# Kernel tuning notes

Hardware: AMD Instinct MI355X
Metric: run time of the kernel (lower is better)

## Reference

```python
import jax, jax.numpy as jnp
import numpy as np

HIDDEN = 1024
HEADS = 16
HEAD_DIM = HIDDEN // HEADS  # 64
B, S = 4, 2048


def setup_inputs() -> dict:
    key = jax.random.key(0)
    ks = jax.random.split(key, 9)
    sd = 1.0 / np.sqrt(HIDDEN)
    return {
        "hidden_state": jax.random.normal(ks[0], (B, S, HIDDEN), dtype=jnp.float32),
        "Wq": jax.random.uniform(ks[1], (HIDDEN, HIDDEN), jnp.float32, -sd, sd),
        "bq": jax.random.uniform(ks[2], (HIDDEN,), jnp.float32, -sd, sd),
        "Wk": jax.random.uniform(ks[3], (HIDDEN, HEAD_DIM), jnp.float32, -sd, sd),
        "bk": jax.random.uniform(ks[4], (HEAD_DIM,), jnp.float32, -sd, sd),
        "Wv": jax.random.uniform(ks[5], (HIDDEN, HEAD_DIM), jnp.float32, -sd, sd),
        "bv": jax.random.uniform(ks[6], (HEAD_DIM,), jnp.float32, -sd, sd),
        "Wo": jax.random.uniform(ks[7], (HIDDEN, HIDDEN), jnp.float32, -sd, sd),
        "bo": jax.random.uniform(ks[8], (HIDDEN,), jnp.float32, -sd, sd),
    }


def reference(hidden_state, Wq, bq, Wk, bk, Wv, bv, Wo, bo):
    b, s, _ = hidden_state.shape
    # projections
    q = hidden_state @ Wq + bq               # [B,S,H*Dh]
    k = hidden_state @ Wk + bk               # [B,S,Dh] (shared across heads)
    v = hidden_state @ Wv + bv               # [B,S,Dh]
    q = q.reshape(b, s, HEADS, HEAD_DIM)     # [B,S,H,Dh]
    scale = 1.0 / jnp.sqrt(jnp.float32(HEAD_DIM))
    # scores: [B,H,S,S] — shared K broadcast over heads via einsum
    scores = jnp.einsum("bqhd,bkd->bhqk", q, k) * scale
    probs = jax.nn.softmax(scores, axis=-1)
    out = jnp.einsum("bhqk,bkd->bqhd", probs, v)  # [B,S,H,Dh]
    out = out.reshape(b, s, HEADS * HEAD_DIM)
    return out @ Wo + bo
```

## Files before the change

kernel.cpp:

```cpp
#include <hip/hip_runtime.h>
#include <hip/hip_bf16.h>
#include <cstdint>

#define HIDDEN 1024
#define HEADS 16
#define HEAD_DIM 64
#define BB 4
#define SS 2048
#define NTOK (BB * SS)

typedef __attribute__((ext_vector_type(8))) __bf16 bf16x8;
typedef __attribute__((ext_vector_type(4))) float f32x4;
typedef unsigned short u16;

#define PSCALE 0.1803368801111137f

__device__ __forceinline__ u16 f2bf(float x) {
    union { float f; uint32_t u; } v; v.f = x;
    uint32_t r = v.u + 0x7FFF + ((v.u >> 16) & 1);
    return (u16)(r >> 16);
}

typedef __attribute__((address_space(3))) uint32_t lds_u32;
typedef __attribute__((address_space(1))) uint32_t glb_u32;
__device__ __forceinline__ void gload16(const u16* g, u16* l) {
    __builtin_amdgcn_global_load_lds((const glb_u32*)g, (lds_u32*)l, 16, 0, 0);
}

__global__ void cvt_f32_bf16(const float* __restrict__ in, u16* __restrict__ out, int n4) {
    int i = blockIdx.x * blockDim.x + threadIdx.x;
    int stride = gridDim.x * blockDim.x;
    for (; i < n4; i += stride) {
        float4 v = ((const float4*)in)[i];
        ushort4 o;
        o.x = f2bf(v.x); o.y = f2bf(v.y); o.z = f2bf(v.z); o.w = f2bf(v.w);
        ((ushort4*)out)[i] = o;
    }
}

__global__ void transpose_to_bf16(const float* __restrict__ W, u16* __restrict__ Wt,
                                  int K, int N) {
    __shared__ float tile[32][33];
    int bx = blockIdx.x;
    int by = blockIdx.y;
    int tx = threadIdx.x;
    int ty = threadIdx.y;
    for (int i = 0; i < 4; i++) {
        int kk = ty + i * 8;
        tile[kk][tx] = W[(size_t)(by * 32 + kk) * N + bx * 32 + tx];
    }
    __syncthreads();
    for (int i = 0; i < 4; i++) {
        int nn = ty + i * 8;
        Wt[(size_t)(bx * 32 + nn) * K + by * 32 + tx] = f2bf(tile[tx][nn]);
    }
}

__global__ __launch_bounds__(256) void gemm128_f32(
    const u16* __restrict__ A, const u16* __restrict__ Bt,
    const float* __restrict__ bias, float* __restrict__ C,
    int M, int N, int K) {
    __shared__ u16 Al[128 * 64];
    __shared__ u16 Bl[128 * 64];
    const int mb = blockIdx.y, nb = blockIdx.x;
    const int tid = threadIdx.x;
    const int w = tid >> 6, lane = tid & 63;
    const int lr = lane & 15, lg = lane >> 4;
    const int wr = w >> 1, wc = w & 1;

    f32x4 acc[4][4] = {};

    const int srow = lane >> 3;
    const int scol = (lane & 7) * 8;
    const u16* Asrc = A + (size_t)(mb * 128 + w * 32 + srow) * K + scol;
    const u16* Bsrc = Bt + (size_t)(nb * 128 + w * 32 + srow) * K + scol;
    u16* Adst = &Al[(w * 32) * 64];
    u16* Bdst = &Bl[(w * 32) * 64];

    for (int k0 = 0; k0 < K; k0 += 64) {
        if (k0) __syncthreads();
#pragma unroll
        for (int i = 0; i < 4; i++) {
            gload16(Asrc + (size_t)(i * 8) * K + k0, Adst + i * 8 * 64);
            gload16(Bsrc + (size_t)(i * 8) * K + k0, Bdst + i * 8 * 64);
        }
        asm volatile("s_waitcnt vmcnt(0)" ::: "memory");
        __syncthreads();

#pragma unroll
        for (int ks = 0; ks < 2; ks++) {
            bf16x8 af[4], bfr[4];
#pragma unroll
            for (int mf = 0; mf < 4; mf++)
                af[mf] = *(const bf16x8*)(&Al[(wr * 64 + mf * 16 + lr) * 64 + ks * 32 + lg * 8]);
#pragma unroll
            for (int nf = 0; nf < 4; nf++)
                bfr[nf] = *(const bf16x8*)(&Bl[(wc * 64 + nf * 16 + lr) * 64 + ks * 32 + lg * 8]);
            __builtin_amdgcn_s_setprio(1);
#pragma unroll
            for (int mf = 0; mf < 4; mf++)
#pragma unroll
                for (int nf = 0; nf < 4; nf++)
                    acc[mf][nf] = __builtin_amdgcn_mfma_f32_16x16x32_bf16(af[mf], bfr[nf], acc[mf][nf], 0, 0, 0);
            __builtin_amdgcn_s_setprio(0);
        }
    }

#pragma unroll
    for (int nf = 0; nf < 4; nf++) {
        int n = nb * 128 + wc * 64 + nf * 16 + lr;
        float bval = bias[n];
#pragma unroll
        for (int mf = 0; mf < 4; mf++)
#pragma unroll
            for (int r = 0; r < 4; r++) {
                int m = mb * 128 + wr * 64 + mf * 16 + lg * 4 + r;
                C[(size_t)m * N + n] = acc[mf][nf][r] + bval;
            }
    }
}

#define NPROJ 1152
__global__ __launch_bounds__(256) void gemm_proj(
    const u16* __restrict__ A, const u16* __restrict__ Bt,
    const float* __restrict__ bq, const float* __restrict__ bk, const float* __restrict__ bv,
    u16* __restrict__ qout, u16* __restrict__ kout, u16* __restrict__ vout) {
    __shared__ u16 Al[128 * 64];
    __shared__ u16 Bl[128 * 64];
    const int mb = blockIdx.y, nb = blockIdx.x;
    const int tid = threadIdx.x;
    const int w = tid >> 6, lane = tid & 63;
    const int lr = lane & 15, lg = lane >> 4;
    const int wr = w >> 1, wc = w & 1;

    f32x4 acc[4][4] = {};

    const int srow = lane >> 3;
    const int scol = (lane & 7) * 8;
    const u16* Asrc = A + (size_t)(mb * 128 + w * 32 + srow) * HIDDEN + scol;
    const u16* Bsrc = Bt + (size_t)(nb * 128 + w * 32 + srow) * HIDDEN + scol;
    u16* Adst = &Al[(w * 32) * 64];
    u16* Bdst = &Bl[(w * 32) * 64];

    for (int k0 = 0; k0 < HIDDEN; k0 += 64) {
        if (k0) __syncthreads();
#pragma unroll
        for (int i = 0; i < 4; i++) {
            gload16(Asrc + (size_t)(i * 8) * HIDDEN + k0, Adst + i * 8 * 64);
            gload16(Bsrc + (size_t)(i * 8) * HIDDEN + k0, Bdst + i * 8 * 64);
        }
        asm volatile("s_waitcnt vmcnt(0)" ::: "memory");
        __syncthreads();

#pragma unroll
        for (int ks = 0; ks < 2; ks++) {
            bf16x8 af[4], bfr[4];
#pragma unroll
            for (int mf = 0; mf < 4; mf++)
                af[mf] = *(const bf16x8*)(&Al[(wr * 64 + mf * 16 + lr) * 64 + ks * 32 + lg * 8]);
#pragma unroll
            for (int nf = 0; nf < 4; nf++)
                bfr[nf] = *(const bf16x8*)(&Bl[(wc * 64 + nf * 16 + lr) * 64 + ks * 32 + lg * 8]);
            __builtin_amdgcn_s_setprio(1);
#pragma unroll
            for (int mf = 0; mf < 4; mf++)
#pragma unroll
                for (int nf = 0; nf < 4; nf++)
                    acc[mf][nf] = __builtin_amdgcn_mfma_f32_16x16x32_bf16(af[mf], bfr[nf], acc[mf][nf], 0, 0, 0);
            __builtin_amdgcn_s_setprio(0);
        }
    }

#pragma unroll
    for (int nf = 0; nf < 4; nf++) {
        int n = nb * 128 + wc * 64 + nf * 16 + lr;
        float bval = (n < 1024) ? bq[n] : (n < 1088) ? bk[n - 1024] : bv[n - 1088];
#pragma unroll
        for (int mf = 0; mf < 4; mf++)
#pragma unroll
            for (int r = 0; r < 4; r++) {
                int m = mb * 128 + wr * 64 + mf * 16 + lg * 4 + r;
                float val = acc[mf][nf][r] + bval;
                if (n < 1024) {
                    qout[(size_t)m * 1024 + n] = f2bf(val * PSCALE);
                } else if (n < 1088) {
                    kout[(size_t)m * 64 + (n - 1024)] = f2bf(val);
                } else {
                    int bb = m >> 11, t = m & (SS - 1);
                    vout[((size_t)bb * 64 + (n - 1088)) * SS + t] = f2bf(val);
                }
            }
    }
}

#define KVB 64
#define NT (SS / KVB)

__global__ __launch_bounds__(512) void attn_kernel(
    const u16* __restrict__ q,
    const u16* __restrict__ k,
    const u16* __restrict__ vt,
    u16* __restrict__ o) {
    const int qt = blockIdx.x, h = blockIdx.y, b = blockIdx.z;
    const int tid = threadIdx.x;
    const int w = tid >> 6, lane = tid & 63;
    const int lr = lane & 15, lg = lane >> 4;

    __shared__ u16 Kl[4][KVB * 64];
    __shared__ u16 Vl[4][KVB * 64];

    const u16* kbase = k + (size_t)b * SS * HEAD_DIM;
    const u16* vbase = vt + (size_t)b * HEAD_DIM * SS;
    const int rowbase = b * SS + qt * 256 + w * 32;

    const int srow = w * 8 + (lane >> 3);
    const int sc16 = (lane & 7) ^ (srow & 7);
    const u16* kp = kbase + (size_t)srow * HEAD_DIM + sc16 * 8;
    const u16* vp = vbase + (size_t)srow * SS + sc16 * 8;

    bf16x8 qf[2][2];
#pragma unroll
    for (int s = 0; s < 2; s++)
#pragma unroll
        for (int ks = 0; ks < 2; ks++)
            qf[s][ks] = *(const bf16x8*)(q + (size_t)(rowbase + s * 16 + lr) * HIDDEN + h * 64 + ks * 32 + lg * 8);

    bf16x8 onesf;
#pragma unroll
    for (int i = 0; i < 8; i++) onesf[i] = (__bf16)1.0f;

    const int xr = lr & 7;
    const int kvro0 = lr * 64 + ((lg) ^ xr) * 8;
    const int kvro1 = lr * 64 + ((4 + lg) ^ xr) * 8;

    f32x4 l_acc[2] = {};
    f32x4 oacc[2][4] = {};

#define VEXP(D, S) asm("v_exp_f32 %0, %1" : "=v"(D) : "v"(S))

#define STAGE(BUF)                            \
    do {                                      \
        gload16(kp, &Kl[BUF][w * 512]);       \
        gload16(vp, &Vl[BUF][w * 512]);       \
        kp += KVB * HEAD_DIM;                 \
        vp += KVB;                            \
    } while (0)

#define CTILE(BUF)                                                                     \
    do {                                                                               \
        f32x4 st0[4] = {}, st1[4] = {};                                                \
        __builtin_amdgcn_s_setprio(1);                                                 \
        _Pragma("unroll") for (int nf = 0; nf < 4; nf++) {                             \
            bf16x8 kf = *(const bf16x8*)(&Kl[BUF][kvro0 + nf * 1024]);                 \
            st0[nf] = __builtin_amdgcn_mfma_f32_16x16x32_bf16(kf, qf[0][0], st0[nf], 0, 0, 0); \
            st1[nf] = __builtin_amdgcn_mfma_f32_16x16x32_bf16(kf, qf[1][0], st1[nf], 0, 0, 0); \
        }                                                                              \
        _Pragma("unroll") for (int nf = 0; nf < 4; nf++) {                             \
            bf16x8 kf = *(const bf16x8*)(&Kl[BUF][kvro1 + nf * 1024]);                 \
            st0[nf] = __builtin_amdgcn_mfma_f32_16x16x32_bf16(kf, qf[0][1], st0[nf], 0, 0, 0); \
            st1[nf] = __builtin_amdgcn_mfma_f32_16x16x32_bf16(kf, qf[1][1], st1[nf], 0, 0, 0); \
        }                                                                              \
        __builtin_amdgcn_s_setprio(0);                                                 \
                      \
        uint32_t c0[8], c1[8];                                                         \
        _Pragma("unroll") for (int nf = 0; nf < 4; nf++) {                             \
            float p0, p1, p2, p3, r0, r1, r2, r3;                                      \
            VEXP(p0, st0[nf][0]); VEXP(p1, st0[nf][1]);                                \
            VEXP(p2, st0[nf][2]); VEXP(p3, st0[nf][3]);                                \
            asm("v_cvt_pk_bf16_f32 %0, %1, %2" : "=v"(c0[nf * 2]) : "v"(p0), "v"(p1)); \
            asm("v_cvt_pk_bf16_f32 %0, %1, %2" : "=v"(c0[nf * 2 + 1]) : "v"(p2), "v"(p3)); \
            VEXP(r0, st1[nf][0]); VEXP(r1, st1[nf][1]);                                \
            VEXP(r2, st1[nf][2]); VEXP(r3, st1[nf][3]);                                \
            asm("v_cvt_pk_bf16_f32 %0, %1, %2" : "=v"(c1[nf * 2]) : "v"(r0), "v"(r1)); \
            asm("v_cvt_pk_bf16_f32 %0, %1, %2" : "=v"(c1[nf * 2 + 1]) : "v"(r2), "v"(r3)); \
        }                                                                              \
                                              \
        _Pragma("unroll") for (int ks = 0; ks < 2; ks++) {                             \
            uint32_t u0 = c0[4 * ks], v0 = c0[4 * ks + 1], x0 = c0[4 * ks + 2], y0 = c0[4 * ks + 3]; \
            uint32_t u1 = c1[4 * ks], v1 = c1[4 * ks + 1], x1 = c1[4 * ks + 2], y1 = c1[4 * ks + 3]; \
            asm("v_permlane32_swap_b32 %0, %1" : "+v"(u0), "+v"(x0));                  \
            asm("v_permlane32_swap_b32 %0, %1" : "+v"(v0), "+v"(y0));                  \
            asm("v_permlane16_swap_b32 %0, %1" : "+v"(u0), "+v"(x0));                  \
            asm("v_permlane16_swap_b32 %0, %1" : "+v"(v0), "+v"(y0));                  \
            asm("v_permlane32_swap_b32 %0, %1" : "+v"(u1), "+v"(x1));                  \
            asm("v_permlane32_swap_b32 %0, %1" : "+v"(v1), "+v"(y1));                  \
            asm("v_permlane16_swap_b32 %0, %1" : "+v"(u1), "+v"(x1));                  \
            asm("v_permlane16_swap_b32 %0, %1" : "+v"(v1), "+v"(y1));                  \
            union { uint32_t wv[4]; bf16x8 v8; } pf0, pf1;                             \
            pf0.wv[0] = u0; pf0.wv[1] = v0; pf0.wv[2] = x0; pf0.wv[3] = y0;            \
            pf1.wv[0] = u1; pf1.wv[1] = v1; pf1.wv[2] = x1; pf1.wv[3] = y1;            \
            const int kvro = ks ? kvro1 : kvro0;                                       \
            __builtin_amdgcn_s_setprio(1);                                             \
            l_acc[0] = __builtin_amdgcn_mfma_f32_16x16x32_bf16(pf0.v8, onesf, l_acc[0], 0, 0, 0); \
            l_acc[1] = __builtin_amdgcn_mfma_f32_16x16x32_bf16(pf1.v8, onesf, l_acc[1], 0, 0, 0); \
            _Pragma("unroll") for (int nf = 0; nf < 4; nf++) {                         \
                bf16x8 vf = *(const bf16x8*)(&Vl[BUF][kvro + nf * 1024]);              \
                oacc[0][nf] = __builtin_amdgcn_mfma_f32_16x16x32_bf16(pf0.v8, vf, oacc[0][nf], 0, 0, 0); \
                oacc[1][nf] = __builtin_amdgcn_mfma_f32_16x16x32_bf16(pf1.v8, vf, oacc[1][nf], 0, 0, 0); \
            }                                                                          \
            __builtin_amdgcn_s_setprio(0);                                             \
        }                                                                              \
    } while (0)

#define STEP(BUFC, DOSTAGE, VM)                                    \
    do {                                                           \
        asm volatile("s_waitcnt vmcnt(" #VM ")" ::: "memory");     \
        __builtin_amdgcn_s_barrier();                              \
        if (DOSTAGE) STAGE(((BUFC) + 3) & 3);                      \
        CTILE(BUFC);                                               \
        asm volatile("" ::: "memory");                             \
    } while (0)

    STAGE(0);
    STAGE(1);
    STAGE(2);

    for (int i = 0; i < 7; i++) {
        STEP(0, 1, 4);
        STEP(1, 1, 4);
        STEP(2, 1, 4);
        STEP(3, 1, 4);
    }
    STEP(0, 1, 4);
    STEP(1, 0, 4);
    STEP(2, 0, 2);
    STEP(3, 0, 0);

#undef STEP
#undef STAGE
#undef CTILE
#undef VEXP

#pragma unroll
    for (int s = 0; s < 2; s++) {
        float li[4];
#pragma unroll
        for (int r = 0; r < 4; r++) li[r] = 1.0f / l_acc[s][r];
#pragma unroll
        for (int nf = 0; nf < 4; nf++)
#pragma unroll
            for (int r = 0; r < 4; r++) {
                float val = oacc[s][nf][r] * li[r];
                o[(size_t)(rowbase + s * 16 + lg * 4 + r) * HIDDEN + h * 64 + nf * 16 + lr] = f2bf(val);
            }
    }
}

extern "C" void kernel_launch(void* const* d_in, const int* in_sizes, int n_in,
                              void* d_out, int out_size, void* d_ws, size_t ws_size,
                              hipStream_t stream) {
    const float* h  = (const float*)d_in[0];
    const float* Wq = (const float*)d_in[1];
    const float* bq = (const float*)d_in[2];
    const float* Wk = (const float*)d_in[3];
    const float* bk = (const float*)d_in[4];
    const float* Wv = (const float*)d_in[5];
    const float* bv = (const float*)d_in[6];
    const float* Wo = (const float*)d_in[7];
    const float* bo = (const float*)d_in[8];

    char* ws = (char*)d_ws;
    u16* hbf  = (u16*)ws; ws += (size_t)NTOK * HIDDEN * 2;
    u16* Wta  = (u16*)ws; ws += (size_t)NPROJ * HIDDEN * 2;
    u16* Wot  = (u16*)ws; ws += (size_t)HIDDEN * HIDDEN * 2;
    u16* qbf  = (u16*)ws; ws += (size_t)NTOK * HIDDEN * 2;
    u16* kbf  = (u16*)ws; ws += (size_t)NTOK * HEAD_DIM * 2;
    u16* vtb  = (u16*)ws; ws += (size_t)NTOK * HEAD_DIM * 2;
    u16* obf  = (u16*)ws; ws += (size_t)NTOK * HIDDEN * 2;

    cvt_f32_bf16<<<2048, 256, 0, stream>>>(h, hbf, NTOK * HIDDEN / 4);
    transpose_to_bf16<<<dim3(HIDDEN / 32, HIDDEN / 32), dim3(32, 8), 0, stream>>>(Wq, Wta, HIDDEN, HIDDEN);
    transpose_to_bf16<<<dim3(HEAD_DIM / 32, HIDDEN / 32), dim3(32, 8), 0, stream>>>(Wk, Wta + (size_t)1024 * HIDDEN, HIDDEN, HEAD_DIM);
    transpose_to_bf16<<<dim3(HEAD_DIM / 32, HIDDEN / 32), dim3(32, 8), 0, stream>>>(Wv, Wta + (size_t)1088 * HIDDEN, HIDDEN, HEAD_DIM);
    transpose_to_bf16<<<dim3(HIDDEN / 32, HIDDEN / 32), dim3(32, 8), 0, stream>>>(Wo, Wot, HIDDEN, HIDDEN);

    gemm_proj<<<dim3(NPROJ / 128, NTOK / 128), 256, 0, stream>>>(hbf, Wta, bq, bk, bv, qbf, kbf, vtb);

    attn_kernel<<<dim3(SS / 256, HEADS, BB), 512, 0, stream>>>(qbf, kbf, vtb, obf);

    gemm128_f32<<<dim3(HIDDEN / 128, NTOK / 128), 256, 0, stream>>>(obf, Wot, bo, (float*)d_out, NTOK, HIDDEN, HIDDEN);
}
```

Before: 152.6 us.

## Pipeline GEMM K-loop with 4-stage LDS ring and swizzled layout

Both GEMM kernels now share a macro-based main loop. It uses a 4-buffer LDS ring with K-step 32, keeps three stages of global-to-LDS loads in flight, and waits on partial vmcnt counts instead of draining after every tile. The LDS layout is XOR-swizzled to cut bank conflicts on the fragment reads. The grid is also transposed so consecutive blocks walk along M, which changes which tiles share L2. The aim is to hide global load latency behind MFMA work, at the cost of more LDS per block and a single barrier per step that relies on the ring depth for safety.

```diff
diff --git a/kernel.cpp b/kernel.cpp
--- a/kernel.cpp
+++ b/kernel.cpp
@@ -56,56 +56,76 @@
     }
 }
 
+
+#define GEMM_PRE()                                                                   \
+    __shared__ u16 Al[4][4096];                                                      \
+    __shared__ u16 Bl[4][4096];                                                      \
+    const int mb = blockIdx.x, nb = blockIdx.y;                                      \
+    const int tid = threadIdx.x;                                                     \
+    const int w = tid >> 6, lane = tid & 63;                                         \
+    const int lr = lane & 15, lg = lane >> 4;                                        \
+    const int wr = w >> 1, wc = w & 1;                                               \
+    f32x4 acc[4][4] = {};                                                            \
+    const int srow4 = lane >> 2;                                                     \
+    const int sg = ((lane & 3) ^ (srow4 & 3)) * 8;                                   \
+    const u16* Ap = A + (size_t)(mb * 128 + w * 32 + srow4) * 1024 + sg;             \
+    const u16* Bp = Bt + (size_t)(nb * 128 + w * 32 + srow4) * 1024 + sg;            \
+    const int aoff = (wr * 64 + lr) * 32 + ((lg ^ (lr & 3)) * 8);                    \
+    const int boff = (wc * 64 + lr) * 32 + ((lg ^ (lr & 3)) * 8);
+
+#define GSTAGE(BUF)                                          \
+    do {                                                     \
+        gload16(Ap, &Al[BUF][w * 1024]);                     \
+        gload16(Ap + 16 * 1024, &Al[BUF][w * 1024 + 512]);   \
+        gload16(Bp, &Bl[BUF][w * 1024]);                     \
+        gload16(Bp + 16 * 1024, &Bl[BUF][w * 1024 + 512]);   \
+        Ap += 32;                                            \
+        Bp += 32;                                            \
+    } while (0)
+
+#define GCOMPUTE(BUF)                                                                \
+    do {                                                                             \
+        bf16x8 af[4], bfr[4];                                                        \
+        _Pragma("unroll") for (int mf = 0; mf < 4; mf++)                             \
+            af[mf] = *(const bf16x8*)(&Al[BUF][aoff + mf * 512]);                    \
+        _Pragma("unroll") for (int nf = 0; nf < 4; nf++)                             \
+            bfr[nf] = *(const bf16x8*)(&Bl[BUF][boff + nf * 512]);                   \
+        __builtin_amdgcn_s_setprio(1);                                               \
+        _Pragma("unroll") for (int mf = 0; mf < 4; mf++)                             \
+            _Pragma("unroll") for (int nf = 0; nf < 4; nf++)                         \
+                acc[mf][nf] = __builtin_amdgcn_mfma_f32_16x16x32_bf16(af[mf], bfr[nf], acc[mf][nf], 0, 0, 0); \
+        __builtin_amdgcn_s_setprio(0);                                               \
+    } while (0)
+
+#define GSTEP(BUFC, DOSTAGE, VM)                                   \
+    do {                                                           \
+        asm volatile("s_waitcnt vmcnt(" #VM ")" ::: "memory");     \
+        __builtin_amdgcn_s_barrier();                              \
+        if (DOSTAGE) GSTAGE(((BUFC) + 3) & 3);                     \
+        GCOMPUTE(BUFC);                                            \
+        asm volatile("" ::: "memory");                             \
+    } while (0)
+
+#define GEMM_LOOP()                                                \
+    GSTAGE(0);                                                     \
+    GSTAGE(1);                                                     \
+    GSTAGE(2);                                                     \
+    for (int i = 0; i < 7; i++) {                                  \
+        GSTEP(0, 1, 8);                                            \
+        GSTEP(1, 1, 8);                                            \
+        GSTEP(2, 1, 8);                                            \
+        GSTEP(3, 1, 8);                                            \
+    }                                                              \
+    GSTEP(0, 1, 8);                                                \
+    GSTEP(1, 0, 8);                                                \
+    GSTEP(2, 0, 4);                                                \
+    GSTEP(3, 0, 0);
+
 __global__ __launch_bounds__(256) void gemm128_f32(
     const u16* __restrict__ A, const u16* __restrict__ Bt,
-    const float* __restrict__ bias, float* __restrict__ C,
-    int M, int N, int K) {
-    __shared__ u16 Al[128 * 64];
-    __shared__ u16 Bl[128 * 64];
-    const int mb = blockIdx.y, nb = blockIdx.x;
-    const int tid = threadIdx.x;
-    const int w = tid >> 6, lane = tid & 63;
-    const int lr = lane & 15, lg = lane >> 4;
-    const int wr = w >> 1, wc = w & 1;
-
-    f32x4 acc[4][4] = {};
-
-    const int srow = lane >> 3;
-    const int scol = (lane & 7) * 8;
-    const u16* Asrc = A + (size_t)(mb * 128 + w * 32 + srow) * K + scol;
-    const u16* Bsrc = Bt + (size_t)(nb * 128 + w * 32 + srow) * K + scol;
-    u16* Adst = &Al[(w * 32) * 64];
-    u16* Bdst = &Bl[(w * 32) * 64];
-
-    for (int k0 = 0; k0 < K; k0 += 64) {
-        if (k0) __syncthreads();
-#pragma unroll
-        for (int i = 0; i < 4; i++) {
-            gload16(Asrc + (size_t)(i * 8) * K + k0, Adst + i * 8 * 64);
-            gload16(Bsrc + (size_t)(i * 8) * K + k0, Bdst + i * 8 * 64);
-        }
-        asm volatile("s_waitcnt vmcnt(0)" ::: "memory");
-        __syncthreads();
-
-#pragma unroll
-        for (int ks = 0; ks < 2; ks++) {
-            bf16x8 af[4], bfr[4];
-#pragma unroll
-            for (int mf = 0; mf < 4; mf++)
-                af[mf] = *(const bf16x8*)(&Al[(wr * 64 + mf * 16 + lr) * 64 + ks * 32 + lg * 8]);
-#pragma unroll
-            for (int nf = 0; nf < 4; nf++)
-                bfr[nf] = *(const bf16x8*)(&Bl[(wc * 64 + nf * 16 + lr) * 64 + ks * 32 + lg * 8]);
-            __builtin_amdgcn_s_setprio(1);
-#pragma unroll
-            for (int mf = 0; mf < 4; mf++)
-#pragma unroll
-                for (int nf = 0; nf < 4; nf++)
-                    acc[mf][nf] = __builtin_amdgcn_mfma_f32_16x16x32_bf16(af[mf], bfr[nf], acc[mf][nf], 0, 0, 0);
-            __builtin_amdgcn_s_setprio(0);
-        }
-    }
-
+    const float* __restrict__ bias, float* __restrict__ C, int N) {
+    GEMM_PRE();
+    GEMM_LOOP();
 #pragma unroll
     for (int nf = 0; nf < 4; nf++) {
         int n = nb * 128 + wc * 64 + nf * 16 + lr;
@@ -120,57 +140,12 @@
     }
 }
 
-#define NPROJ 1152
 __global__ __launch_bounds__(256) void gemm_proj(
     const u16* __restrict__ A, const u16* __restrict__ Bt,
     const float* __restrict__ bq, const float* __restrict__ bk, const float* __restrict__ bv,
     u16* __restrict__ qout, u16* __restrict__ kout, u16* __restrict__ vout) {
-    __shared__ u16 Al[128 * 64];
-    __shared__ u16 Bl[128 * 64];
-    const int mb = blockIdx.y, nb = blockIdx.x;
-    const int tid = threadIdx.x;
-    const int w = tid >> 6, lane = tid & 63;
-    const int lr = lane & 15, lg = lane >> 4;
-    const int wr = w >> 1, wc = w & 1;
-
-    f32x4 acc[4][4] = {};
-
-    const int srow = lane >> 3;
-    const int scol = (lane & 7) * 8;
-    const u16* Asrc = A + (size_t)(mb * 128 + w * 32 + srow) * HIDDEN + scol;
-    const u16* Bsrc = Bt + (size_t)(nb * 128 + w * 32 + srow) * HIDDEN + scol;
-    u16* Adst = &Al[(w * 32) * 64];
-    u16* Bdst = &Bl[(w * 32) * 64];
-
-    for (int k0 = 0; k0 < HIDDEN; k0 += 64) {
-        if (k0) __syncthreads();
-#pragma unroll
-        for (int i = 0; i < 4; i++) {
-            gload16(Asrc + (size_t)(i * 8) * HIDDEN + k0, Adst + i * 8 * 64);
-            gload16(Bsrc + (size_t)(i * 8) * HIDDEN + k0, Bdst + i * 8 * 64);
-        }
-        asm volatile("s_waitcnt vmcnt(0)" ::: "memory");
-        __syncthreads();
-
-#pragma unroll
-        for (int ks = 0; ks < 2; ks++) {
-            bf16x8 af[4], bfr[4];
-#pragma unroll
-            for (int mf = 0; mf < 4; mf++)
-                af[mf] = *(const bf16x8*)(&Al[(wr * 64 + mf * 16 + lr) * 64 + ks * 32 + lg * 8]);
-#pragma unroll
-            for (int nf = 0; nf < 4; nf++)
-                bfr[nf] = *(const bf16x8*)(&Bl[(wc * 64 + nf * 16 + lr) * 64 + ks * 32 + lg * 8]);
-            __builtin_amdgcn_s_setprio(1);
-#pragma unroll
-            for (int mf = 0; mf < 4; mf++)
-#pragma unroll
-                for (int nf = 0; nf < 4; nf++)
-                    acc[mf][nf] = __builtin_amdgcn_mfma_f32_16x16x32_bf16(af[mf], bfr[nf], acc[mf][nf], 0, 0, 0);
-            __builtin_amdgcn_s_setprio(0);
-        }
-    }
-
+    GEMM_PRE();
+    GEMM_LOOP();
 #pragma unroll
     for (int nf = 0; nf < 4; nf++) {
         int n = nb * 128 + wc * 64 + nf * 16 + lr;
@@ -361,7 +336,7 @@
 
     char* ws = (char*)d_ws;
     u16* hbf  = (u16*)ws; ws += (size_t)NTOK * HIDDEN * 2;
-    u16* Wta  = (u16*)ws; ws += (size_t)NPROJ * HIDDEN * 2;
+    u16* Wta  = (u16*)ws; ws += (size_t)1152 * HIDDEN * 2;
     u16* Wot  = (u16*)ws; ws += (size_t)HIDDEN * HIDDEN * 2;
     u16* qbf  = (u16*)ws; ws += (size_t)NTOK * HIDDEN * 2;
     u16* kbf  = (u16*)ws; ws += (size_t)NTOK * HEAD_DIM * 2;
@@ -374,9 +349,9 @@
     transpose_to_bf16<<<dim3(HEAD_DIM / 32, HIDDEN / 32), dim3(32, 8), 0, stream>>>(Wv, Wta + (size_t)1088 * HIDDEN, HIDDEN, HEAD_DIM);
     transpose_to_bf16<<<dim3(HIDDEN / 32, HIDDEN / 32), dim3(32, 8), 0, stream>>>(Wo, Wot, HIDDEN, HIDDEN);
 
-    gemm_proj<<<dim3(NPROJ / 128, NTOK / 128), 256, 0, stream>>>(hbf, Wta, bq, bk, bv, qbf, kbf, vtb);
+    gemm_proj<<<dim3(NTOK / 128, 1152 / 128), 256, 0, stream>>>(hbf, Wta, bq, bk, bv, qbf, kbf, vtb);
 
     attn_kernel<<<dim3(SS / 256, HEADS, BB), 512, 0, stream>>>(qbf, kbf, vtb, obf);
 
-    gemm128_f32<<<dim3(HIDDEN / 128, NTOK / 128), 256, 0, stream>>>(obf, Wot, bo, (float*)d_out, NTOK, HIDDEN, HIDDEN);
-}
+    gemm128_f32<<<dim3(NTOK / 128, HIDDEN / 128), 256, 0, stream>>>(obf, Wot, bo, (float*)d_out, HIDDEN);
+}
```

New measurement: 162.2 us. +6.3%, slower.

## Software-pipeline attention loop (PV of tile i with QK/exp of i+1) and merge transposes

Applied to the files above, without the earlier changes.

Splits the attention tile body into a QK^T+exp stage and a PV accumulation stage, then reorders the loop so the PV MFMAs for the previous tile are issued alongside the QK and exp work of the next tile. This hides exp and permute latency behind matrix work. The stage/wait schedule is adjusted to match. Separately, the four weight-transpose launches are merged into one 3D-grid launch to cut launch overhead. The cost is 16 extra live registers for the carried probabilities, which could reduce occupancy.

```diff
diff --git a/kernel.cpp b/kernel.cpp
--- a/kernel.cpp
+++ b/kernel.cpp
@@ -38,21 +38,28 @@
     }
 }
 
-__global__ void transpose_to_bf16(const float* __restrict__ W, u16* __restrict__ Wt,
-                                  int K, int N) {
+__global__ void transpose4_to_bf16(const float* __restrict__ Wq, const float* __restrict__ Wk,
+                                   const float* __restrict__ Wv, const float* __restrict__ Wo,
+                                   u16* __restrict__ Wta, u16* __restrict__ Wot) {
     __shared__ float tile[32][33];
-    int bx = blockIdx.x;
-    int by = blockIdx.y;
-    int tx = threadIdx.x;
-    int ty = threadIdx.y;
+    const int z = blockIdx.z;
+    const int Nz = (z == 1 || z == 2) ? 64 : 1024;
+    const int bx = blockIdx.x;
+    if (bx * 32 >= Nz) return;
+    const float* W = (z == 0) ? Wq : (z == 1) ? Wk : (z == 2) ? Wv : Wo;
+    u16* Wt = (z == 0) ? Wta : (z == 1) ? (Wta + (size_t)1024 * HIDDEN)
+              : (z == 2) ? (Wta + (size_t)1088 * HIDDEN) : Wot;
+    const int by = blockIdx.y;
+    const int tx = threadIdx.x;
+    const int ty = threadIdx.y;
     for (int i = 0; i < 4; i++) {
         int kk = ty + i * 8;
-        tile[kk][tx] = W[(size_t)(by * 32 + kk) * N + bx * 32 + tx];
+        tile[kk][tx] = W[(size_t)(by * 32 + kk) * Nz + bx * 32 + tx];
     }
     __syncthreads();
     for (int i = 0; i < 4; i++) {
         int nn = ty + i * 8;
-        Wt[(size_t)(bx * 32 + nn) * K + by * 32 + tx] = f2bf(tile[tx][nn]);
+        Wt[(size_t)(bx * 32 + nn) * 1024 + by * 32 + tx] = f2bf(tile[tx][nn]);
     }
 }
 
@@ -235,6 +242,7 @@
 
     f32x4 l_acc[2] = {};
     f32x4 oacc[2][4] = {};
+    uint32_t pw[16];
 
 #define VEXP(D, S) asm("v_exp_f32 %0, %1" : "=v"(D) : "v"(S))
 
@@ -246,7 +254,7 @@
         vp += KVB;                            \
     } while (0)
 
-#define CTILE(BUF)                                                                     \
+#define QKEXP(BUF)                                                                     \
     do {                                                                               \
         f32x4 st0[4] = {}, st1[4] = {};                                                \
         __builtin_amdgcn_s_setprio(1);                                                 \
@@ -261,7 +269,6 @@
             st1[nf] = __builtin_amdgcn_mfma_f32_16x16x32_bf16(kf, qf[1][1], st1[nf], 0, 0, 0); \
         }                                                                              \
         __builtin_amdgcn_s_setprio(0);                                                 \
-                      \
         uint32_t c0[8], c1[8];                                                         \
         _Pragma("unroll") for (int nf = 0; nf < 4; nf++) {                             \
             float p0, p1, p2, p3, r0, r1, r2, r3;                                      \
@@ -274,7 +281,6 @@
             asm("v_cvt_pk_bf16_f32 %0, %1, %2" : "=v"(c1[nf * 2]) : "v"(r0), "v"(r1)); \
             asm("v_cvt_pk_bf16_f32 %0, %1, %2" : "=v"(c1[nf * 2 + 1]) : "v"(r2), "v"(r3)); \
         }                                                                              \
-                                              \
         _Pragma("unroll") for (int ks = 0; ks < 2; ks++) {                             \
             uint32_t u0 = c0[4 * ks], v0 = c0[4 * ks + 1], x0 = c0[4 * ks + 2], y0 = c0[4 * ks + 3]; \
             uint32_t u1 = c1[4 * ks], v1 = c1[4 * ks + 1], x1 = c1[4 * ks + 2], y1 = c1[4 * ks + 3]; \
@@ -286,11 +292,23 @@
             asm("v_permlane32_swap_b32 %0, %1" : "+v"(v1), "+v"(y1));                  \
             asm("v_permlane16_swap_b32 %0, %1" : "+v"(u1), "+v"(x1));                  \
             asm("v_permlane16_swap_b32 %0, %1" : "+v"(v1), "+v"(y1));                  \
-            union { uint32_t wv[4]; bf16x8 v8; } pf0, pf1;                             \
-            pf0.wv[0] = u0; pf0.wv[1] = v0; pf0.wv[2] = x0; pf0.wv[3] = y0;            \
-            pf1.wv[0] = u1; pf1.wv[1] = v1; pf1.wv[2] = x1; pf1.wv[3] = y1;            \
+            pw[ks * 4 + 0] = u0; pw[ks * 4 + 1] = v0;                                  \
+            pw[ks * 4 + 2] = x0; pw[ks * 4 + 3] = y0;                                  \
+            pw[8 + ks * 4 + 0] = u1; pw[8 + ks * 4 + 1] = v1;                          \
+            pw[8 + ks * 4 + 2] = x1; pw[8 + ks * 4 + 3] = y1;                          \
+        }                                                                              \
+    } while (0)
+
+#define PVACC(BUF)                                                                     \
+    do {                                                                               \
+        union { uint32_t wv[4]; bf16x8 v8; } pf0, pf1;                                 \
+        __builtin_amdgcn_s_setprio(1);                                                 \
+        _Pragma("unroll") for (int ks = 0; ks < 2; ks++) {                             \
+            pf0.wv[0] = pw[ks * 4 + 0]; pf0.wv[1] = pw[ks * 4 + 1];                    \
+            pf0.wv[2] = pw[ks * 4 + 2]; pf0.wv[3] = pw[ks * 4 + 3];                    \
+            pf1.wv[0] = pw[8 + ks * 4 + 0]; pf1.wv[1] = pw[8 + ks * 4 + 1];            \
+            pf1.wv[2] = pw[8 + ks * 4 + 2]; pf1.wv[3] = pw[8 + ks * 4 + 3];            \
             const int kvro = ks ? kvro1 : kvro0;                                       \
-            __builtin_amdgcn_s_setprio(1);                                             \
             l_acc[0] = __builtin_amdgcn_mfma_f32_16x16x32_bf16(pf0.v8, onesf, l_acc[0], 0, 0, 0); \
             l_acc[1] = __builtin_amdgcn_mfma_f32_16x16x32_bf16(pf1.v8, onesf, l_acc[1], 0, 0, 0); \
             _Pragma("unroll") for (int nf = 0; nf < 4; nf++) {                         \
@@ -298,37 +316,42 @@
                 oacc[0][nf] = __builtin_amdgcn_mfma_f32_16x16x32_bf16(pf0.v8, vf, oacc[0][nf], 0, 0, 0); \
                 oacc[1][nf] = __builtin_amdgcn_mfma_f32_16x16x32_bf16(pf1.v8, vf, oacc[1][nf], 0, 0, 0); \
             }                                                                          \
-            __builtin_amdgcn_s_setprio(0);                                             \
         }                                                                              \
+        __builtin_amdgcn_s_setprio(0);                                                 \
     } while (0)
 
-#define STEP(BUFC, DOSTAGE, VM)                                    \
+#define ITER(BPV, BQK, BST, DOSTAGE, VM)                           \
     do {                                                           \
         asm volatile("s_waitcnt vmcnt(" #VM ")" ::: "memory");     \
         __builtin_amdgcn_s_barrier();                              \
-        if (DOSTAGE) STAGE(((BUFC) + 3) & 3);                      \
-        CTILE(BUFC);                                               \
+        if (DOSTAGE) STAGE(BST);                                   \
+        PVACC(BPV);                                                \
+        QKEXP(BQK);                                                \
         asm volatile("" ::: "memory");                             \
     } while (0)
 
     STAGE(0);
     STAGE(1);
+    asm volatile("s_waitcnt vmcnt(2)" ::: "memory");
+    __builtin_amdgcn_s_barrier();
     STAGE(2);
+    QKEXP(0);
 
     for (int i = 0; i < 7; i++) {
-        STEP(0, 1, 4);
-        STEP(1, 1, 4);
-        STEP(2, 1, 4);
-        STEP(3, 1, 4);
-    }
-    STEP(0, 1, 4);
-    STEP(1, 0, 4);
-    STEP(2, 0, 2);
-    STEP(3, 0, 0);
-
-#undef STEP
+        ITER(0, 1, 3, 1, 2);
+        ITER(1, 2, 0, 1, 2);
+        ITER(2, 3, 1, 1, 2);
+        ITER(3, 0, 2, 1, 2);
+    }
+    ITER(0, 1, 3, 1, 2);
+    ITER(1, 2, 3, 0, 2);
+    ITER(2, 3, 3, 0, 0);
+    PVACC(3);
+
+#undef ITER
 #undef STAGE
-#undef CTILE
+#undef QKEXP
+#undef PVACC
 #undef VEXP
 
 #pragma unroll
@@ -369,10 +392,7 @@
     u16* obf  = (u16*)ws; ws += (size_t)NTOK * HIDDEN * 2;
 
     cvt_f32_bf16<<<2048, 256, 0, stream>>>(h, hbf, NTOK * HIDDEN / 4);
-    transpose_to_bf16<<<dim3(HIDDEN / 32, HIDDEN / 32), dim3(32, 8), 0, stream>>>(Wq, Wta, HIDDEN, HIDDEN);
-    transpose_to_bf16<<<dim3(HEAD_DIM / 32, HIDDEN / 32), dim3(32, 8), 0, stream>>>(Wk, Wta + (size_t)1024 * HIDDEN, HIDDEN, HEAD_DIM);
-    transpose_to_bf16<<<dim3(HEAD_DIM / 32, HIDDEN / 32), dim3(32, 8), 0, stream>>>(Wv, Wta + (size_t)1088 * HIDDEN, HIDDEN, HEAD_DIM);
-    transpose_to_bf16<<<dim3(HIDDEN / 32, HIDDEN / 32), dim3(32, 8), 0, stream>>>(Wo, Wot, HIDDEN, HIDDEN);
+    transpose4_to_bf16<<<dim3(32, 32, 4), dim3(32, 8), 0, stream>>>(Wq, Wk, Wv, Wo, Wta, Wot);
 
     gemm_proj<<<dim3(NPROJ / 128, NTOK / 128), 256, 0, stream>>>(hbf, Wta, bq, bk, bv, qbf, kbf, vtb);
 
```

Result: faster. 146.1 us (median of 2 runs) (-4.2%).
